# Kernel tuning notes

Hardware: AMD Instinct MI355X
Metric: run time of the kernel (lower is better)

Reference implementation:

```python
import jax, jax.numpy as jnp
import numpy as np

N_NODES = 50000

def _gcn_conv(x, W, b, src, dst, num_nodes):
    # PyG GCNConv: linear transform, then D^{-1/2} A_hat D^{-1/2} aggregation (A_hat has self-loops).
    xw = x @ W                                   # [N, out]
    ones = jnp.ones(src.shape[0], dtype=x.dtype)
    deg = jax.ops.segment_sum(ones, dst, num_segments=num_nodes)  # in-degree incl. self loop
    dinv = jnp.where(deg > 0, jax.lax.rsqrt(deg), 0.0)
    norm = dinv[src] * dinv[dst]                 # [E]
    msg = xw[src] * norm[:, None]                # [E, out] gather + scale
    out = jax.ops.segment_sum(msg, dst, num_segments=num_nodes)   # scatter-add
    return out + b

def _add_self_loops(edge_index, num_nodes):
    loop = jnp.arange(num_nodes, dtype=edge_index.dtype)
    src = jnp.concatenate([edge_index[0], loop])
    dst = jnp.concatenate([edge_index[1], loop])
    return src, dst

def setup_inputs() -> dict:
    key = jax.random.key(0)
    k = jax.random.split(key, 6)
    in_dim, hid_dim, out_dim = 256, 128, 64
    n_edges = 800000
    x = jax.random.normal(k[0], (N_NODES, in_dim), dtype=jnp.float32)
    edge_index = jax.random.randint(k[1], (2, n_edges), 0, N_NODES, dtype=jnp.int64)
    W1 = jax.random.normal(k[2], (in_dim, hid_dim), dtype=jnp.float32) / np.sqrt(in_dim)
    b1 = jnp.zeros((hid_dim,), dtype=jnp.float32)
    W2 = jax.random.normal(k[3], (hid_dim, out_dim), dtype=jnp.float32) / np.sqrt(hid_dim)
    b2 = jnp.zeros((out_dim,), dtype=jnp.float32)
    return {"x": x, "edge_index": edge_index, "W1": W1, "b1": b1, "W2": W2, "b2": b2}

def reference(x, edge_index, W1, b1, W2, b2):
    src, dst = _add_self_loops(edge_index, N_NODES)
    h = jnp.tanh(_gcn_conv(x, W1, b1, src, dst, N_NODES))
    out = _gcn_conv(h, W2, b2, src, dst, N_NODES)
    return out
```

## Files before the change

kernel.cpp:

```cpp
#include <hip/hip_runtime.h>

#define INDIM 256
#define HID 128
#define OUTD 64

typedef _Float16 f16x8 __attribute__((ext_vector_type(8)));
typedef float    f32x4 __attribute__((ext_vector_type(4)));


__global__ __launch_bounds__(256) void k_zero2(int* __restrict__ a, int* __restrict__ b, int n) {
    int i = blockIdx.x * 256 + threadIdx.x;
    if (i < n) { a[i] = 0; b[i] = 0; }
}

__global__ __launch_bounds__(256) void k_count(const int* __restrict__ dst, int* __restrict__ counts, int E) {
    int e = blockIdx.x * 256 + threadIdx.x;
    if (e < E) atomicAdd(&counts[dst[e]], 1);
}

__global__ __launch_bounds__(256) void k_breduce(const int* __restrict__ counts, int* __restrict__ bsum, int M) {
    __shared__ int s[256];
    int tid = threadIdx.x;
    int i = blockIdx.x * 256 + tid;
    s[tid] = (i < M) ? counts[i] : 0;
    __syncthreads();
#pragma unroll
    for (int off = 128; off > 0; off >>= 1) {
        if (tid < off) s[tid] += s[tid + off];
        __syncthreads();
    }
    if (tid == 0) bsum[blockIdx.x] = s[0];
}

__global__ __launch_bounds__(256) void k_bscan(int* __restrict__ bsum, int NB) {
    __shared__ int s[256];
    int tid = threadIdx.x;
    int v = (tid < NB) ? bsum[tid] : 0;
    s[tid] = v;
    __syncthreads();
#pragma unroll
    for (int off = 1; off < 256; off <<= 1) {
        int t = (tid >= off) ? s[tid - off] : 0;
        __syncthreads();
        s[tid] += t;
        __syncthreads();
    }
    if (tid < NB) bsum[tid] = s[tid] - v;
}

__global__ __launch_bounds__(256) void k_scan_final(const int* __restrict__ counts, const int* __restrict__ bsum,
                                                    int* __restrict__ row_start, float* __restrict__ dinv, int M) {
    __shared__ int s[256];
    int tid = threadIdx.x;
    int i = blockIdx.x * 256 + tid;
    int v = (i < M) ? counts[i] : 0;
    s[tid] = v;
    __syncthreads();
#pragma unroll
    for (int off = 1; off < 256; off <<= 1) {
        int t = (tid >= off) ? s[tid - off] : 0;
        __syncthreads();
        s[tid] += t;
        __syncthreads();
    }
    if (i < M) {
        int excl = bsum[blockIdx.x] + s[tid] - v;
        row_start[i] = excl;
        dinv[i] = rsqrtf(1.0f + (float)v);
        if (i == M - 1) row_start[M] = excl + v;
    }
}

__global__ __launch_bounds__(256) void k_fill(const int* __restrict__ src, const int* __restrict__ dst,
                                              const int* __restrict__ row_start, int* __restrict__ cursor,
                                              const float* __restrict__ dinv,
                                              int2* __restrict__ edges, int E) {
    int e = blockIdx.x * 256 + threadIdx.x;
    if (e >= E) return;
    int s = src[e], d = dst[e];
    int pos = row_start[d] + atomicAdd(&cursor[d], 1);
    edges[pos] = make_int2(s, __float_as_int(dinv[s] * dinv[d]));
}

__global__ __launch_bounds__(256) void k_prepw(const float* __restrict__ W, _Float16* __restrict__ Wt,
                                               int K, int N) {
    int id = blockIdx.x * 256 + threadIdx.x;
    if (id < N * K) {
        int n = id / K, k = id % K;
        Wt[id] = (_Float16)W[k * N + n];
    }
}

template <int BN, int K, typename AT>
__global__ __launch_bounds__(256) void k_gemm_mfma(
    const AT* __restrict__ X, const _Float16* __restrict__ Wt,
    _Float16* __restrict__ XW16, int M)
{
    constexpr int BM = 64;
    constexpr int BK = 32;
    constexpr int NT = BN / 16;
    constexpr int LDK = BK + 8;

    __shared__ __align__(16) _Float16 As[BM][LDK];
    __shared__ __align__(16) _Float16 Bs[BN][LDK];

    const int tid  = threadIdx.x;
    const int wave = tid >> 6;
    const int lane = tid & 63;
    const int m    = lane & 15;
    const int q    = lane >> 4;
    const int rb   = blockIdx.x * BM;

    f32x4 acc[NT];
#pragma unroll
    for (int t = 0; t < NT; t++) acc[t] = (f32x4){0.f, 0.f, 0.f, 0.f};

    for (int kt = 0; kt < K; kt += BK) {
        if (kt) __syncthreads();
        if constexpr (sizeof(AT) == 4) {
#pragma unroll
            for (int i = 0; i < BM * 8 / 256; i++) {
                int ch  = tid + i * 256;
                int row = ch >> 3;
                int c4  = ch & 7;
                int gr  = rb + row;
                float4 v = make_float4(0.f, 0.f, 0.f, 0.f);
                if (gr < M) v = *(const float4*)((const float*)X + (long)gr * K + kt + c4 * 4);
                _Float16* p = &As[row][c4 * 4];
                p[0] = (_Float16)v.x; p[1] = (_Float16)v.y;
                p[2] = (_Float16)v.z; p[3] = (_Float16)v.w;
            }
        } else {
            int row = tid >> 2;
            int c8  = tid & 3;
            int gr  = rb + row;
            uint4 v = make_uint4(0u, 0u, 0u, 0u);
            if (gr < M) v = *(const uint4*)((const _Float16*)X + (long)gr * K + kt + c8 * 8);
            *(uint4*)(&As[row][c8 * 8]) = v;
        }
#pragma unroll
        for (int i = 0; i < BN * 8 / 256; i++) {
            int ch = tid + i * 256;
            int n  = ch >> 3;
            int c4 = ch & 7;
            *(ushort4*)(&Bs[n][c4 * 4]) =
                *(const ushort4*)(Wt + (long)n * K + kt + c4 * 4);
        }
        __syncthreads();

        f16x8 af = *(const f16x8*)(&As[wave * 16 + m][q * 8]);
#pragma unroll
        for (int t = 0; t < NT; t++) {
            f16x8 bf = *(const f16x8*)(&Bs[t * 16 + m][q * 8]);
            acc[t] = __builtin_amdgcn_mfma_f32_16x16x32_f16(af, bf, acc[t], 0, 0, 0);
        }
    }

    int row0 = rb + wave * 16 + q * 4;
#pragma unroll
    for (int r = 0; r < 4; r++) {
        int row = row0 + r;
        if (row < M) {
#pragma unroll
            for (int t = 0; t < NT; t++) {
                XW16[(long)row * BN + t * 16 + m] = (_Float16)acc[t][r];
            }
        }
    }
}

template <int F, bool TANH, typename OutT>
__global__ __launch_bounds__(256) void k_agg_csr(const int* __restrict__ row_start,
                                                 const int2* __restrict__ edges,
                                                 const _Float16* __restrict__ feat,
                                                 const float* __restrict__ bias,
                                                 const float* __restrict__ dinv,
                                                 OutT* __restrict__ out, int M) {
    constexpr int LPN = F / 8;
    constexpr int NPB = 256 / LPN;
    int n = blockIdx.x * NPB + threadIdx.x / LPN;
    int c = threadIdx.x % LPN;
    if (n >= M) return;
    int beg = row_start[n], end = row_start[n + 1];
    float di  = dinv[n];
    float di2 = di * di;

    f16x8 self = *(const f16x8*)(feat + (long)n * F + c * 8);
    float acc[8];
#pragma unroll
    for (int k = 0; k < 8; k++) acc[k] = bias[c * 8 + k] + (float)self[k] * di2;

    for (int j = beg; j < end; j++) {
        int2 e  = edges[j];
        float w = __int_as_float(e.y);
        f16x8 v = *(const f16x8*)(feat + (long)e.x * F + c * 8);
#pragma unroll
        for (int k = 0; k < 8; k++) acc[k] += (float)v[k] * w;
    }
    if (TANH) {
#pragma unroll
        for (int k = 0; k < 8; k++) acc[k] = tanhf(acc[k]);
    }
    if constexpr (sizeof(OutT) == 2) {
        f16x8 o;
#pragma unroll
        for (int k = 0; k < 8; k++) o[k] = (_Float16)acc[k];
        *(f16x8*)((_Float16*)out + (long)n * F + c * 8) = o;
    } else {
        float* p = (float*)out + (long)n * F + c * 8;
        *(float4*)(p)     = make_float4(acc[0], acc[1], acc[2], acc[3]);
        *(float4*)(p + 4) = make_float4(acc[4], acc[5], acc[6], acc[7]);
    }
}

extern "C" void kernel_launch(void* const* d_in, const int* in_sizes, int n_in,
                              void* d_out, int out_size, void* d_ws, size_t ws_size,
                              hipStream_t stream) {
    const float* x  = (const float*)d_in[0];
    const int*   ei = (const int*)d_in[1];
    const float* W1 = (const float*)d_in[2];
    const float* b1 = (const float*)d_in[3];
    const float* W2 = (const float*)d_in[4];
    const float* b2 = (const float*)d_in[5];
    float* out = (float*)d_out;

    const int M = in_sizes[0] / INDIM;
    const int E = in_sizes[1] / 2;
    const int* srcp = ei;
    const int* dstp = ei + E;

    const int Mp = (M + 63) & ~63;
    const int NB = (M + 255) / 256;

    float*     dinv      = (float*)d_ws;
    int*       counts    = (int*)(dinv + Mp);
    int*       cursor    = counts + Mp;
    int*       row_start = cursor + Mp;
    int*       bsum      = row_start + Mp;
    _Float16*  W1t       = (_Float16*)(bsum + 256);
    _Float16*  W2t       = W1t + HID * INDIM;
    int2*      edges     = (int2*)(W2t + OUTD * HID);
    _Float16*  xw16      = (_Float16*)(edges + E);
    _Float16*  h16       = xw16 + (long)M * HID;
    _Float16*  hw16      = xw16;

    k_prepw<<<(HID * INDIM + 255) / 256, 256, 0, stream>>>(W1, W1t, INDIM, HID);
    k_prepw<<<(OUTD * HID + 255) / 256, 256, 0, stream>>>(W2, W2t, HID, OUTD);

    k_zero2<<<(M + 255) / 256, 256, 0, stream>>>(counts, cursor, M);
    k_count<<<(E + 255) / 256, 256, 0, stream>>>(dstp, counts, E);
    k_breduce<<<NB, 256, 0, stream>>>(counts, bsum, M);
    k_bscan<<<1, 256, 0, stream>>>(bsum, NB);
    k_scan_final<<<NB, 256, 0, stream>>>(counts, bsum, row_start, dinv, M);
    k_fill<<<(E + 255) / 256, 256, 0, stream>>>(srcp, dstp, row_start, cursor, dinv, edges, E);

    k_gemm_mfma<HID, INDIM, float><<<(M + 63) / 64, 256, 0, stream>>>(x, W1t, xw16, M);
    k_agg_csr<HID, true, _Float16><<<(M + 15) / 16, 256, 0, stream>>>(row_start, edges, xw16, b1, dinv, h16, M);

    k_gemm_mfma<OUTD, HID, _Float16><<<(M + 63) / 64, 256, 0, stream>>>(h16, W2t, hw16, M);
    k_agg_csr<OUTD, false, float><<<(M + 31) / 32, 256, 0, stream>>>(row_start, edges, hw16, b2, dinv, out, M);
}
```

Before: 271.9 us.

## Fold symmetric normalization into GEMM epilogue and drop per-edge weights

Factors the D^{-1/2} A D^{-1/2} normalization: the GEMM epilogue pre-scales each row by dinv[src], and the aggregation multiplies the summed neighbors by dinv[dst]. The CSR then stores only source indices (4 bytes per edge instead of 8), which removes the dinv gathers in k_fill and halves edge traffic in both aggregations. The aggregation loop is unrolled by two, and the weight-prep and zeroing kernels are merged into one launch. Pre-scaled features are stored in fp16 before summation, which slightly changes rounding.

After: 254.6 us. -6.3%, faster.

```diff
diff --git a/kernel.cpp b/kernel.cpp
--- a/kernel.cpp
+++ b/kernel.cpp
@@ -7,11 +7,25 @@
 typedef _Float16 f16x8 __attribute__((ext_vector_type(8)));
 typedef float    f32x4 __attribute__((ext_vector_type(4)));
 
-
-__global__ __launch_bounds__(256) void k_zero2(int* __restrict__ a, int* __restrict__ b, int n) {
-    int i = blockIdx.x * 256 + threadIdx.x;
-    if (i < n) { a[i] = 0; b[i] = 0; }
-}
+__global__ __launch_bounds__(256) void k_setup(const float* __restrict__ W1, const float* __restrict__ W2,
+                                               _Float16* __restrict__ W1t, _Float16* __restrict__ W2t,
+                                               int* __restrict__ counts, int* __restrict__ cursor, int M) {
+    constexpr int NW1 = HID * INDIM;
+    constexpr int NW2 = OUTD * HID;
+    int id = blockIdx.x * 256 + threadIdx.x;
+    if (id < NW1) {
+        int n = id / INDIM, k = id % INDIM;
+        W1t[id] = (_Float16)W1[k * HID + n];
+    } else if (id < NW1 + NW2) {
+        int j = id - NW1;
+        int n = j / HID, k = j % HID;
+        W2t[j] = (_Float16)W2[k * OUTD + n];
+    } else {
+        int i = id - NW1 - NW2;
+        if (i < M) { counts[i] = 0; cursor[i] = 0; }
+    }
+}
+
 
 __global__ __launch_bounds__(256) void k_count(const int* __restrict__ dst, int* __restrict__ counts, int E) {
     int e = blockIdx.x * 256 + threadIdx.x;
@@ -73,28 +87,18 @@
 
 __global__ __launch_bounds__(256) void k_fill(const int* __restrict__ src, const int* __restrict__ dst,
                                               const int* __restrict__ row_start, int* __restrict__ cursor,
-                                              const float* __restrict__ dinv,
-                                              int2* __restrict__ edges, int E) {
+                                              int* __restrict__ edge_src, int E) {
     int e = blockIdx.x * 256 + threadIdx.x;
     if (e >= E) return;
-    int s = src[e], d = dst[e];
+    int d = dst[e];
     int pos = row_start[d] + atomicAdd(&cursor[d], 1);
-    edges[pos] = make_int2(s, __float_as_int(dinv[s] * dinv[d]));
-}
-
-__global__ __launch_bounds__(256) void k_prepw(const float* __restrict__ W, _Float16* __restrict__ Wt,
-                                               int K, int N) {
-    int id = blockIdx.x * 256 + threadIdx.x;
-    if (id < N * K) {
-        int n = id / K, k = id % K;
-        Wt[id] = (_Float16)W[k * N + n];
-    }
+    edge_src[pos] = src[e];
 }
 
 template <int BN, int K, typename AT>
 __global__ __launch_bounds__(256) void k_gemm_mfma(
     const AT* __restrict__ X, const _Float16* __restrict__ Wt,
-    _Float16* __restrict__ XW16, int M)
+    const float* __restrict__ dinv, _Float16* __restrict__ XW16, int M)
 {
     constexpr int BM = 64;
     constexpr int BK = 32;
@@ -161,9 +165,10 @@
     for (int r = 0; r < 4; r++) {
         int row = row0 + r;
         if (row < M) {
+            float di = dinv[row];
 #pragma unroll
             for (int t = 0; t < NT; t++) {
-                XW16[(long)row * BN + t * 16 + m] = (_Float16)acc[t][r];
+                XW16[(long)row * BN + t * 16 + m] = (_Float16)(acc[t][r] * di);
             }
         }
     }
@@ -171,7 +176,7 @@
 
 template <int F, bool TANH, typename OutT>
 __global__ __launch_bounds__(256) void k_agg_csr(const int* __restrict__ row_start,
-                                                 const int2* __restrict__ edges,
+                                                 const int* __restrict__ edge_src,
                                                  const _Float16* __restrict__ feat,
                                                  const float* __restrict__ bias,
                                                  const float* __restrict__ dinv,
@@ -182,21 +187,30 @@
     int c = threadIdx.x % LPN;
     if (n >= M) return;
     int beg = row_start[n], end = row_start[n + 1];
-    float di  = dinv[n];
-    float di2 = di * di;
 
     f16x8 self = *(const f16x8*)(feat + (long)n * F + c * 8);
     float acc[8];
 #pragma unroll
-    for (int k = 0; k < 8; k++) acc[k] = bias[c * 8 + k] + (float)self[k] * di2;
-
-    for (int j = beg; j < end; j++) {
-        int2 e  = edges[j];
-        float w = __int_as_float(e.y);
-        f16x8 v = *(const f16x8*)(feat + (long)e.x * F + c * 8);
-#pragma unroll
-        for (int k = 0; k < 8; k++) acc[k] += (float)v[k] * w;
-    }
+    for (int k = 0; k < 8; k++) acc[k] = (float)self[k];
+
+    int j = beg;
+    for (; j + 1 < end; j += 2) {
+        int s0 = edge_src[j], s1 = edge_src[j + 1];
+        f16x8 v0 = *(const f16x8*)(feat + (long)s0 * F + c * 8);
+        f16x8 v1 = *(const f16x8*)(feat + (long)s1 * F + c * 8);
+#pragma unroll
+        for (int k = 0; k < 8; k++) acc[k] += (float)v0[k] + (float)v1[k];
+    }
+    if (j < end) {
+        int s = edge_src[j];
+        f16x8 v = *(const f16x8*)(feat + (long)s * F + c * 8);
+#pragma unroll
+        for (int k = 0; k < 8; k++) acc[k] += (float)v[k];
+    }
+
+    float di = dinv[n];
+#pragma unroll
+    for (int k = 0; k < 8; k++) acc[k] = bias[c * 8 + k] + di * acc[k];
     if (TANH) {
 #pragma unroll
         for (int k = 0; k < 8; k++) acc[k] = tanhf(acc[k]);
@@ -239,24 +253,25 @@
     int*       bsum      = row_start + Mp;
     _Float16*  W1t       = (_Float16*)(bsum + 256);
     _Float16*  W2t       = W1t + HID * INDIM;
-    int2*      edges     = (int2*)(W2t + OUTD * HID);
-    _Float16*  xw16      = (_Float16*)(edges + E);
+    int*       edge_src  = (int*)(W2t + OUTD * HID);
+    _Float16*  xw16      = (_Float16*)(edge_src + E);
     _Float16*  h16       = xw16 + (long)M * HID;
     _Float16*  hw16      = xw16;
 
-    k_prepw<<<(HID * INDIM + 255) / 256, 256, 0, stream>>>(W1, W1t, INDIM, HID);
-    k_prepw<<<(OUTD * HID + 255) / 256, 256, 0, stream>>>(W2, W2t, HID, OUTD);
-
-    k_zero2<<<(M + 255) / 256, 256, 0, stream>>>(counts, cursor, M);
+    {
+        int total = HID * INDIM + OUTD * HID + M;
+        k_setup<<<(total + 255) / 256, 256, 0, stream>>>(W1, W2, W1t, W2t, counts, cursor, M);
+    }
+
     k_count<<<(E + 255) / 256, 256, 0, stream>>>(dstp, counts, E);
     k_breduce<<<NB, 256, 0, stream>>>(counts, bsum, M);
     k_bscan<<<1, 256, 0, stream>>>(bsum, NB);
     k_scan_final<<<NB, 256, 0, stream>>>(counts, bsum, row_start, dinv, M);
-    k_fill<<<(E + 255) / 256, 256, 0, stream>>>(srcp, dstp, row_start, cursor, dinv, edges, E);
-
-    k_gemm_mfma<HID, INDIM, float><<<(M + 63) / 64, 256, 0, stream>>>(x, W1t, xw16, M);
-    k_agg_csr<HID, true, _Float16><<<(M + 15) / 16, 256, 0, stream>>>(row_start, edges, xw16, b1, dinv, h16, M);
-
-    k_gemm_mfma<OUTD, HID, _Float16><<<(M + 63) / 64, 256, 0, stream>>>(h16, W2t, hw16, M);
-    k_agg_csr<OUTD, false, float><<<(M + 31) / 32, 256, 0, stream>>>(row_start, edges, hw16, b2, dinv, out, M);
-}
+    k_fill<<<(E + 255) / 256, 256, 0, stream>>>(srcp, dstp, row_start, cursor, edge_src, E);
+
+    k_gemm_mfma<HID, INDIM, float><<<(M + 63) / 64, 256, 0, stream>>>(x, W1t, dinv, xw16, M);
+    k_agg_csr<HID, true, _Float16><<<(M + 15) / 16, 256, 0, stream>>>(row_start, edge_src, xw16, b1, dinv, h16, M);
+
+    k_gemm_mfma<OUTD, HID, _Float16><<<(M + 63) / 64, 256, 0, stream>>>(h16, W2t, dinv, hw16, M);
+    k_agg_csr<OUTD, false, float><<<(M + 31) / 32, 256, 0, stream>>>(row_start, edge_src, hw16, b2, dinv, out, M);
+}
```
